# Kernel optimization log

Measured on AMD Instinct MI355X. Metric: run time of the kernel, lower is better.

## Reference

```python
import jax, jax.numpy as jnp
import numpy as np

N_EMBD = 1024
N_HEAD = 16

def setup_inputs() -> dict:
    key = jax.random.key(0)
    k1, k2, k3 = jax.random.split(key, 3)
    x = jax.random.normal(k1, (2, 2048, N_EMBD), dtype=jnp.float32)
    # torch Linear(n, 3n): y = x @ W_attn (we store transposed weight directly)
    w_attn = jax.random.normal(k2, (N_EMBD, 3 * N_EMBD), dtype=jnp.float32) * 0.02
    w_proj = jax.random.normal(k3, (N_EMBD, N_EMBD), dtype=jnp.float32) * 0.02
    return {"x": x, "w_attn": w_attn, "w_proj": w_proj}

def reference(x, w_attn, w_proj):
    B, S, E = x.shape
    H = N_HEAD
    D = E // H
    qkv = x @ w_attn  # [B, S, 3E]
    q, k, v = jnp.split(qkv, 3, axis=-1)
    # [B, H, S, D]
    q = q.reshape(B, S, H, D).transpose(0, 2, 1, 3)
    k = k.reshape(B, S, H, D).transpose(0, 2, 1, 3)
    v = v.reshape(B, S, H, D).transpose(0, 2, 1, 3)
    scale = 1.0 / jnp.sqrt(jnp.asarray(D, dtype=x.dtype))
    a = jnp.einsum('bhqd,bhkd->bhqk', q, k) * scale  # [B, H, S, S]
    causal = jnp.tril(jnp.ones((S, S), dtype=bool))
    a = jnp.where(causal, a, -jnp.inf)
    a = jax.nn.softmax(a, axis=-1)
    y = jnp.einsum('bhqk,bhkd->bhqd', a, v)  # [B, H, S, D]
    y = y.transpose(0, 2, 1, 3).reshape(B, S, E)
    return y @ w_proj
```

## Files before the change

kernel.cpp:

```cpp
#include <hip/hip_runtime.h>

#define DEVI __device__ __forceinline__

typedef short bf16x8 __attribute__((ext_vector_type(8)));
typedef float f32x4 __attribute__((ext_vector_type(4)));
typedef unsigned short u16;
typedef unsigned int u32;

static constexpr int Bn = 2, S = 2048, E = 1024, H = 16, D = 64;
static constexpr int Mrows = Bn * S;
static constexpr int N_QKV = 3 * E;

DEVI u16 f2b(float f) {
  union { float f; u32 u; } c; c.f = f;
  return (u16)((c.u + 0x7FFFu + ((c.u >> 16) & 1u)) >> 16);
}

DEVI bf16x8 ld8(const u16* p) {
  union { uint4 u; bf16x8 v; } c;
  c.u = *reinterpret_cast<const uint4*>(p);
  return c.v;
}

#define MFMA(a, b, c) __builtin_amdgcn_mfma_f32_16x16x32_bf16(a, b, c, 0, 0, 0)

#define G2L16(gptr, lptr) \
  __builtin_amdgcn_global_load_lds((const __attribute__((address_space(1))) void*)(gptr), \
                                   (__attribute__((address_space(3))) void*)(lptr), 16, 0, 0)

__global__ __launch_bounds__(256) void prep(const float* __restrict__ x,
                                            const float* __restrict__ w_attn,
                                            const float* __restrict__ w_proj,
                                            u16* __restrict__ xb, u16* __restrict__ wabT,
                                            u16* __restrict__ wpbT) {
  __shared__ float t[32][33];
  int blk = blockIdx.x, tid = threadIdx.x;
  if (blk >= 4096) {
    int i = (blk - 4096) * 256 + tid;
    float4 f = reinterpret_cast<const float4*>(x)[i];
    ushort4 u;
    u.x = f2b(f.x); u.y = f2b(f.y); u.z = f2b(f.z); u.w = f2b(f.w);
    reinterpret_cast<ushort4*>(xb)[i] = u;
    return;
  }
  const float* in; u16* out; int R, C, bx, by;
  if (blk < 3072) {
    in = w_attn; out = wabT; R = E; C = N_QKV;
    bx = (blk % 96) * 32; by = (blk / 96) * 32;
  } else {
    int q = blk - 3072;
    in = w_proj; out = wpbT; R = E; C = E;
    bx = (q % 32) * 32; by = (q / 32) * 32;
  }
  int tx = tid & 31, ty = tid >> 5;
#pragma unroll
  for (int k = 0; k < 32; k += 8)
    t[ty + k][tx] = in[(size_t)(by + ty + k) * C + bx + tx];
  __syncthreads();
#pragma unroll
  for (int k = 0; k < 32; k += 8)
    out[(size_t)(bx + ty + k) * R + by + tx] = f2b(t[tx][ty + k]);
}

__global__ __launch_bounds__(256) void gemm_qkv(const u16* __restrict__ A, const u16* __restrict__ BT,
                                                u16* __restrict__ Qb, u16* __restrict__ Kb,
                                                u16* __restrict__ VbT) {
  constexpr int K = 1024, BK = 64;
  __shared__ __align__(16) u16 As[128 * BK];
  __shared__ __align__(16) u16 Bs[64 * BK];
  int tid = threadIdx.x;
  int w = tid >> 6, lane = tid & 63, quad = lane >> 4, l15 = lane & 15;
  int m0 = blockIdx.x * 128, n0 = blockIdx.y * 64;
  int mw = (w >> 1) * 64, nw = (w & 1) * 32;
  const u16* Ab = A + (size_t)m0 * K;
  const u16* Bb = BT + (size_t)n0 * K;
  f32x4 acc[4][2] = {};
  for (int k0 = 0; k0 < K; k0 += BK) {
#pragma unroll
    for (int j = 0; j < 4; j++) {
      int L = j * 256 + tid;
      int row = L >> 3, cg = (L & 7) ^ (row & 7);
      G2L16(Ab + (size_t)row * K + k0 + cg * 8, (char*)As + L * 16);
    }
#pragma unroll
    for (int j = 0; j < 2; j++) {
      int L = j * 256 + tid;
      int row = L >> 3, cg = (L & 7) ^ (row & 7);
      G2L16(Bb + (size_t)row * K + k0 + cg * 8, (char*)Bs + L * 16);
    }
    __syncthreads();
#pragma unroll
    for (int kk = 0; kk < 2; kk++) {
      int sg = ((kk << 2) | quad) ^ (l15 & 7);
      bf16x8 a[4], b[2];
#pragma unroll
      for (int i = 0; i < 4; i++) a[i] = ld8(&As[(mw + i * 16 + l15) * BK + sg * 8]);
#pragma unroll
      for (int i = 0; i < 2; i++) b[i] = ld8(&Bs[(nw + i * 16 + l15) * BK + sg * 8]);
#pragma unroll
      for (int mb = 0; mb < 4; mb++)
#pragma unroll
        for (int nb = 0; nb < 2; nb++)
          acc[mb][nb] = MFMA(a[mb], b[nb], acc[mb][nb]);
    }
    __syncthreads();
  }
#pragma unroll
  for (int mb = 0; mb < 4; mb++) {
    int m = m0 + mw + mb * 16 + quad * 4;
    int b = m >> 11, s = m & 2047;
#pragma unroll
    for (int nb = 0; nb < 2; nb++) {
      int n = n0 + nw + nb * 16 + l15;
      int sec = n >> 10, e = n & 1023, h = e >> 6, d = e & 63;
      int bh = b * H + h;
      if (sec == 0) {
#pragma unroll
        for (int r = 0; r < 4; r++)
          Qb[((size_t)bh * S + s + r) * D + d] = f2b(acc[mb][nb][r] * 0.125f);
      } else if (sec == 1) {
#pragma unroll
        for (int r = 0; r < 4; r++)
          Kb[((size_t)bh * S + s + r) * D + d] = f2b(acc[mb][nb][r]);
      } else {
        ushort4 v;
        v.x = f2b(acc[mb][nb][0]); v.y = f2b(acc[mb][nb][1]);
        v.z = f2b(acc[mb][nb][2]); v.w = f2b(acc[mb][nb][3]);
        *reinterpret_cast<ushort4*>(VbT + ((size_t)bh * D + d) * S + s) = v;
      }
    }
  }
}

__global__ __launch_bounds__(256, 3) void attn(const u16* __restrict__ Qb, const u16* __restrict__ Kb,
                                               const u16* __restrict__ VbT, u16* __restrict__ Yb) {
  __shared__ __align__(16) u16 Ks[128 * 64];
  __shared__ __align__(16) u16 Vs[64 * 128];
  __shared__ __align__(16) u32 Ps[4][16 * 68];
  int w = threadIdx.x >> 6, lane = threadIdx.x & 63, quad = lane >> 4, l15 = lane & 15;
  int bh = blockIdx.x & 31, p = blockIdx.x >> 5;
  int b = bh >> 4, h = bh & 15;
  int qtA = 31 - p, qtB = p;
  int ncA = (qtA + 2) >> 1, ncB = (qtB + 2) >> 1;

  const u16* Kbh = Kb + (size_t)bh * S * D;
  const u16* Vbh = VbT + (size_t)bh * D * S;
  u32* myP = &Ps[w][0];
  const u16* myP16 = (const u16*)myP;
  int prow = l15 * 68 + quad * 2;

  int qbA = qtA * 64 + w * 16, qbB = qtB * 64 + w * 16;
  int kmaxA = qbA + 16, kmaxB = qbB + 16;
  const u16* QpA = Qb + ((size_t)bh * S + qbA + l15) * D + quad * 8;
  const u16* QpB = Qb + ((size_t)bh * S + qbB + l15) * D + quad * 8;
  bf16x8 bqA0 = ld8(QpA), bqA1 = ld8(QpA + 32);
  bf16x8 bqB0 = ld8(QpB), bqB1 = ld8(QpB + 32);

  float lA = 0.f, lB = 0.f;
  f32x4 oA[4] = {}, oB[4] = {};
  int kbase = 0;

  auto process = [&](int q_base, int kmaxW, bf16x8 bq0, bf16x8 bq1, f32x4* o, float& lpart) {
#pragma unroll
    for (int mb = 0; mb < 8; mb++) {
      int kb = kbase + mb * 16;
      u32 pa = 0, pb = 0;
      if (kb < kmaxW) {
        int row = mb * 16 + l15;
        bf16x8 ak0 = ld8(&Ks[row * 64 + ((quad ^ (row & 7)) * 8)]);
        bf16x8 ak1 = ld8(&Ks[row * 64 + (((quad + 4) ^ (row & 7)) * 8)]);
        f32x4 z = {};
        z = MFMA(ak0, bq0, z);
        z = MFMA(ak1, bq1, z);
        if (kb == q_base) {
#pragma unroll
          for (int r = 0; r < 4; r++)
            if (quad * 4 + r > l15) z[r] = -1e30f;
        }
        float p0 = __expf(z[0]), p1 = __expf(z[1]);
        float p2 = __expf(z[2]), p3 = __expf(z[3]);
        lpart += (p0 + p1) + (p2 + p3);
        pa = (u32)f2b(p0) | ((u32)f2b(p1) << 16);
        pb = (u32)f2b(p2) | ((u32)f2b(p3) << 16);
      }
      uint2 pw; pw.x = pa; pw.y = pb;
      *reinterpret_cast<uint2*>(&myP[prow + mb * 8]) = pw;
    }
#pragma unroll
    for (int ch = 0; ch < 4; ch++) {
      if (kbase + ch * 32 < kmaxW) {
        bf16x8 bp = ld8(myP16 + l15 * 136 + ch * 32 + quad * 8);
#pragma unroll
        for (int dd = 0; dd < 4; dd++) {
          int rv = dd * 16 + l15;
          bf16x8 av = ld8(&Vs[rv * 128 + (((ch * 4 + quad) ^ (rv & 15)) * 8)]);
          o[dd] = MFMA(av, bp, o[dd]);
        }
      }
    }
  };

  for (int c = 0; c < ncA; c++) {
    kbase = c * 128;
    __syncthreads();
    const u16* Kg = Kbh + (size_t)kbase * D;
#pragma unroll
    for (int j = 0; j < 4; j++) {
      int L = (w * 4 + j) * 64 + lane;
      int row = L >> 3, cg = (L & 7) ^ (row & 7);
      G2L16(Kg + (size_t)row * 64 + cg * 8, (char*)Ks + L * 16);
    }
    const u16* Vg = Vbh + kbase;
#pragma unroll
    for (int j = 0; j < 4; j++) {
      int L = (w * 4 + j) * 64 + lane;
      int row = L >> 4, cg = (L & 15) ^ (row & 15);
      G2L16(Vg + (size_t)row * S + cg * 8, (char*)Vs + L * 16);
    }
    __syncthreads();

    process(qbA, kmaxA, bqA0, bqA1, oA, lA);
    if (c < ncB)
      process(qbB, kmaxB, bqB0, bqB1, oB, lB);
  }

  {
    float l = lA; l += __shfl_xor(l, 16); l += __shfl_xor(l, 32);
    float rinv = 1.0f / l;
    u16* Yp = Yb + ((size_t)b * S + qbA + l15) * E + h * 64 + quad * 4;
#pragma unroll
    for (int dd = 0; dd < 4; dd++) {
      ushort4 y;
      y.x = f2b(oA[dd][0] * rinv); y.y = f2b(oA[dd][1] * rinv);
      y.z = f2b(oA[dd][2] * rinv); y.w = f2b(oA[dd][3] * rinv);
      *reinterpret_cast<ushort4*>(Yp + dd * 16) = y;
    }
  }
  {
    float l = lB; l += __shfl_xor(l, 16); l += __shfl_xor(l, 32);
    float rinv = 1.0f / l;
    u16* Yp = Yb + ((size_t)b * S + qbB + l15) * E + h * 64 + quad * 4;
#pragma unroll
    for (int dd = 0; dd < 4; dd++) {
      ushort4 y;
      y.x = f2b(oB[dd][0] * rinv); y.y = f2b(oB[dd][1] * rinv);
      y.z = f2b(oB[dd][2] * rinv); y.w = f2b(oB[dd][3] * rinv);
      *reinterpret_cast<ushort4*>(Yp + dd * 16) = y;
    }
  }
}

__global__ __launch_bounds__(256) void gemm_proj(const u16* __restrict__ A, const u16* __restrict__ BT,
                                                 float* __restrict__ out) {
  constexpr int K = 1024, BK = 64;
  __shared__ __align__(16) u16 As[128 * BK];
  __shared__ __align__(16) u16 Bs[64 * BK];
  int tid = threadIdx.x;
  int w = tid >> 6, lane = tid & 63, quad = lane >> 4, l15 = lane & 15;
  int m0 = blockIdx.x * 128, n0 = blockIdx.y * 64;
  int mw = (w >> 1) * 64, nw = (w & 1) * 32;
  const u16* Ab = A + (size_t)m0 * K;
  const u16* Bb = BT + (size_t)n0 * K;
  f32x4 acc[4][2] = {};
  for (int k0 = 0; k0 < K; k0 += BK) {
#pragma unroll
    for (int j = 0; j < 4; j++) {
      int L = j * 256 + tid;
      int row = L >> 3, cg = (L & 7) ^ (row & 7);
      G2L16(Ab + (size_t)row * K + k0 + cg * 8, (char*)As + L * 16);
    }
#pragma unroll
    for (int j = 0; j < 2; j++) {
      int L = j * 256 + tid;
      int row = L >> 3, cg = (L & 7) ^ (row & 7);
      G2L16(Bb + (size_t)row * K + k0 + cg * 8, (char*)Bs + L * 16);
    }
    __syncthreads();
#pragma unroll
    for (int kk = 0; kk < 2; kk++) {
      int sg = ((kk << 2) | quad) ^ (l15 & 7);
      bf16x8 a[4], b[2];
#pragma unroll
      for (int i = 0; i < 4; i++) a[i] = ld8(&As[(mw + i * 16 + l15) * BK + sg * 8]);
#pragma unroll
      for (int i = 0; i < 2; i++) b[i] = ld8(&Bs[(nw + i * 16 + l15) * BK + sg * 8]);
#pragma unroll
      for (int mb = 0; mb < 4; mb++)
#pragma unroll
        for (int nb = 0; nb < 2; nb++)
          acc[mb][nb] = MFMA(a[mb], b[nb], acc[mb][nb]);
    }
    __syncthreads();
  }
#pragma unroll
  for (int mb = 0; mb < 4; mb++) {
    int m = m0 + mw + mb * 16 + quad * 4;
#pragma unroll
    for (int nb = 0; nb < 2; nb++) {
      int n = n0 + nw + nb * 16 + l15;
#pragma unroll
      for (int r = 0; r < 4; r++)
        out[(size_t)(m + r) * E + n] = acc[mb][nb][r];
    }
  }
}

extern "C" void kernel_launch(void* const* d_in, const int* in_sizes, int n_in,
                              void* d_out, int out_size, void* d_ws, size_t ws_size,
                              hipStream_t stream) {
  const float* x = (const float*)d_in[0];
  const float* w_attn = (const float*)d_in[1];
  const float* w_proj = (const float*)d_in[2];
  float* out = (float*)d_out;
  char* ws = (char*)d_ws;

  u16* xb   = (u16*)(ws);
  u16* wabT = (u16*)(ws + 8388608);
  u16* wpbT = (u16*)(ws + 14680064);
  u16* Qb   = (u16*)(ws + 16777216);
  u16* Kb   = (u16*)(ws + 25165824);
  u16* VbT  = (u16*)(ws + 33554432);
  u16* Yb   = (u16*)(ws + 41943040);

  prep<<<8192, 256, 0, stream>>>(x, w_attn, w_proj, xb, wabT, wpbT);
  gemm_qkv<<<dim3(Mrows / 128, N_QKV / 64), 256, 0, stream>>>(xb, wabT, Qb, Kb, VbT);
  attn<<<Bn * H * (S / 128), 256, 0, stream>>>(Qb, Kb, VbT, Yb);
  gemm_proj<<<dim3(Mrows / 128, E / 64), 256, 0, stream>>>(Yb, wpbT, out);
}
```

Baseline: 171.5 us.

## Interleave paired query tiles sharing K/V fragment loads, use exp2 and cheaper bf16 packing

Merges the two per-tile passes over each K/V chunk into one loop, so the K fragments and V fragments loaded from LDS are reused for both the A and B query tiles. It also gives each tile its own P buffer. The softmax switches to exp2 by folding log2(e) into the Q scale, and bf16 rounding becomes a simple add-and-perm (round-half-up rather than round-to-even). Occupancy is lowered from 3 to 2 blocks per CU to make room for the extra registers and LDS, which may reduce latency hiding.

```diff
diff --git a/kernel.cpp b/kernel.cpp
--- a/kernel.cpp
+++ b/kernel.cpp
@@ -117,7 +117,7 @@
       if (sec == 0) {
 #pragma unroll
         for (int r = 0; r < 4; r++)
-          Qb[((size_t)bh * S + s + r) * D + d] = f2b(acc[mb][nb][r] * 0.125f);
+          Qb[((size_t)bh * S + s + r) * D + d] = f2b(acc[mb][nb][r] * 0.1803368801111244f);
       } else if (sec == 1) {
 #pragma unroll
         for (int r = 0; r < 4; r++)
@@ -132,11 +132,12 @@
   }
 }
 
-__global__ __launch_bounds__(256, 3) void attn(const u16* __restrict__ Qb, const u16* __restrict__ Kb,
+__global__ __launch_bounds__(256, 2) void attn(const u16* __restrict__ Qb, const u16* __restrict__ Kb,
                                                const u16* __restrict__ VbT, u16* __restrict__ Yb) {
   __shared__ __align__(16) u16 Ks[128 * 64];
   __shared__ __align__(16) u16 Vs[64 * 128];
-  __shared__ __align__(16) u32 Ps[4][16 * 68];
+  __shared__ __align__(16) u32 PsA[4][16 * 68];
+  __shared__ __align__(16) u32 PsB[4][16 * 68];
   int w = threadIdx.x >> 6, lane = threadIdx.x & 63, quad = lane >> 4, l15 = lane & 15;
   int bh = blockIdx.x & 31, p = blockIdx.x >> 5;
   int b = bh >> 4, h = bh & 15;
@@ -145,8 +146,10 @@
 
   const u16* Kbh = Kb + (size_t)bh * S * D;
   const u16* Vbh = VbT + (size_t)bh * D * S;
-  u32* myP = &Ps[w][0];
-  const u16* myP16 = (const u16*)myP;
+  u32* myPA = &PsA[w][0];
+  u32* myPB = &PsB[w][0];
+  const u16* myPA16 = (const u16*)myPA;
+  const u16* myPB16 = (const u16*)myPB;
   int prow = l15 * 68 + quad * 2;
 
   int qbA = qtA * 64 + w * 16, qbB = qtB * 64 + w * 16;
@@ -158,50 +161,10 @@
 
   float lA = 0.f, lB = 0.f;
   f32x4 oA[4] = {}, oB[4] = {};
-  int kbase = 0;
-
-  auto process = [&](int q_base, int kmaxW, bf16x8 bq0, bf16x8 bq1, f32x4* o, float& lpart) {
-#pragma unroll
-    for (int mb = 0; mb < 8; mb++) {
-      int kb = kbase + mb * 16;
-      u32 pa = 0, pb = 0;
-      if (kb < kmaxW) {
-        int row = mb * 16 + l15;
-        bf16x8 ak0 = ld8(&Ks[row * 64 + ((quad ^ (row & 7)) * 8)]);
-        bf16x8 ak1 = ld8(&Ks[row * 64 + (((quad + 4) ^ (row & 7)) * 8)]);
-        f32x4 z = {};
-        z = MFMA(ak0, bq0, z);
-        z = MFMA(ak1, bq1, z);
-        if (kb == q_base) {
-#pragma unroll
-          for (int r = 0; r < 4; r++)
-            if (quad * 4 + r > l15) z[r] = -1e30f;
-        }
-        float p0 = __expf(z[0]), p1 = __expf(z[1]);
-        float p2 = __expf(z[2]), p3 = __expf(z[3]);
-        lpart += (p0 + p1) + (p2 + p3);
-        pa = (u32)f2b(p0) | ((u32)f2b(p1) << 16);
-        pb = (u32)f2b(p2) | ((u32)f2b(p3) << 16);
-      }
-      uint2 pw; pw.x = pa; pw.y = pb;
-      *reinterpret_cast<uint2*>(&myP[prow + mb * 8]) = pw;
-    }
-#pragma unroll
-    for (int ch = 0; ch < 4; ch++) {
-      if (kbase + ch * 32 < kmaxW) {
-        bf16x8 bp = ld8(myP16 + l15 * 136 + ch * 32 + quad * 8);
-#pragma unroll
-        for (int dd = 0; dd < 4; dd++) {
-          int rv = dd * 16 + l15;
-          bf16x8 av = ld8(&Vs[rv * 128 + (((ch * 4 + quad) ^ (rv & 15)) * 8)]);
-          o[dd] = MFMA(av, bp, o[dd]);
-        }
-      }
-    }
-  };
 
   for (int c = 0; c < ncA; c++) {
-    kbase = c * 128;
+    int kbase = c * 128;
+    bool doB = (c < ncB);
     __syncthreads();
     const u16* Kg = Kbh + (size_t)kbase * D;
 #pragma unroll
@@ -219,9 +182,77 @@
     }
     __syncthreads();
 
-    process(qbA, kmaxA, bqA0, bqA1, oA, lA);
-    if (c < ncB)
-      process(qbB, kmaxB, bqB0, bqB1, oB, lB);
+#pragma unroll
+    for (int mb = 0; mb < 8; mb++) {
+      int kb = kbase + mb * 16;
+      u32 pa = 0, pb = 0, pc = 0, pd = 0;
+      if (kb < kmaxA) {
+        int row = mb * 16 + l15;
+        bf16x8 ak0 = ld8(&Ks[row * 64 + ((quad ^ (row & 7)) * 8)]);
+        bf16x8 ak1 = ld8(&Ks[row * 64 + (((quad + 4) ^ (row & 7)) * 8)]);
+        f32x4 zA = {};
+        zA = MFMA(ak0, bqA0, zA);
+        zA = MFMA(ak1, bqA1, zA);
+        if (kb == qbA) {
+#pragma unroll
+          for (int r = 0; r < 4; r++)
+            if (quad * 4 + r > l15) zA[r] = -1e30f;
+        }
+        float a0 = __builtin_amdgcn_exp2f(zA[0]);
+        float a1 = __builtin_amdgcn_exp2f(zA[1]);
+        float a2 = __builtin_amdgcn_exp2f(zA[2]);
+        float a3 = __builtin_amdgcn_exp2f(zA[3]);
+        lA += (a0 + a1) + (a2 + a3);
+        union { float f; u32 u; } u0, u1, u2, u3;
+        u0.f = a0; u1.f = a1; u2.f = a2; u3.f = a3;
+        pa = __builtin_amdgcn_perm(u1.u + 0x8000u, u0.u + 0x8000u, 0x07060302u);
+        pb = __builtin_amdgcn_perm(u3.u + 0x8000u, u2.u + 0x8000u, 0x07060302u);
+        if (doB && kb < kmaxB) {
+          f32x4 zB = {};
+          zB = MFMA(ak0, bqB0, zB);
+          zB = MFMA(ak1, bqB1, zB);
+          if (kb == qbB) {
+#pragma unroll
+            for (int r = 0; r < 4; r++)
+              if (quad * 4 + r > l15) zB[r] = -1e30f;
+          }
+          float b0 = __builtin_amdgcn_exp2f(zB[0]);
+          float b1 = __builtin_amdgcn_exp2f(zB[1]);
+          float b2 = __builtin_amdgcn_exp2f(zB[2]);
+          float b3 = __builtin_amdgcn_exp2f(zB[3]);
+          lB += (b0 + b1) + (b2 + b3);
+          union { float f; u32 u; } v0, v1, v2, v3;
+          v0.f = b0; v1.f = b1; v2.f = b2; v3.f = b3;
+          pc = __builtin_amdgcn_perm(v1.u + 0x8000u, v0.u + 0x8000u, 0x07060302u);
+          pd = __builtin_amdgcn_perm(v3.u + 0x8000u, v2.u + 0x8000u, 0x07060302u);
+        }
+      }
+      uint2 pwA; pwA.x = pa; pwA.y = pb;
+      *reinterpret_cast<uint2*>(&myPA[prow + mb * 8]) = pwA;
+      if (doB) {
+        uint2 pwB; pwB.x = pc; pwB.y = pd;
+        *reinterpret_cast<uint2*>(&myPB[prow + mb * 8]) = pwB;
+      }
+    }
+#pragma unroll
+    for (int ch = 0; ch < 4; ch++) {
+      if (kbase + ch * 32 < kmaxA) {
+        bf16x8 bpA = ld8(myPA16 + l15 * 136 + ch * 32 + quad * 8);
+        bf16x8 av[4];
+#pragma unroll
+        for (int dd = 0; dd < 4; dd++) {
+          int rv = dd * 16 + l15;
+          av[dd] = ld8(&Vs[rv * 128 + (((ch * 4 + quad) ^ (rv & 15)) * 8)]);
+        }
+#pragma unroll
+        for (int dd = 0; dd < 4; dd++) oA[dd] = MFMA(av[dd], bpA, oA[dd]);
+        if (doB && kbase + ch * 32 < kmaxB) {
+          bf16x8 bpB = ld8(myPB16 + l15 * 136 + ch * 32 + quad * 8);
+#pragma unroll
+          for (int dd = 0; dd < 4; dd++) oB[dd] = MFMA(av[dd], bpB, oB[dd]);
+        }
+      }
+    }
   }
 
   {
```

After: 167.9 us. 2.1% less time.
